# Optimization experiments

Hardware: AMD Instinct MI355X
Metric: run time of the kernel (lower is better)

## Reference

```python
import jax, jax.numpy as jnp
import numpy as np

H_STEP = 0.01  # Rosenbrock step size h


def phi_1_pade(A):
    """Pade(1,1) approximation of phi_1(z) = (e^z - 1)/z.

    phi_1(z) ~ (1 + z/6) / (1 - z/3), applied as a matrix function:
    (I - A/3)^{-1} (I + A/6). A: [..., d, d].
    """
    d = A.shape[-1]
    I = jnp.eye(d, dtype=A.dtype)
    return jnp.linalg.solve(I - A / 3.0, I + A / 6.0)


def setup_inputs() -> dict:
    key = jax.random.key(0)
    k_y, k_w1, k_w2 = jax.random.split(key, 3)
    B, D, HID = 512, 256, 1024
    y = jax.random.normal(k_y, (B, D), jnp.float32)
    W1 = jax.random.normal(k_w1, (HID, D), jnp.float32) / np.float32(np.sqrt(D))
    b1 = jnp.zeros((HID,), jnp.float32)
    W2 = jax.random.normal(k_w2, (D, HID), jnp.float32) / np.float32(np.sqrt(HID))
    b2 = jnp.zeros((D,), jnp.float32)
    return {"y": y, "W1": W1, "b1": b1, "W2": W2, "b2": b2}


def reference(y, W1, b1, W2, b2):
    dim = W2.shape[0]  # state dimension d

    def f(y_mu):  # SDE drift: 2-layer tanh MLP, R^d -> R^d
        return W2 @ jnp.tanh(W1 @ y_mu + b1) + b2

    def jac_and_val(y_mu):
        # jacfwd with aux: Jacobian and function value in one forward pass
        jac, val = jax.jacfwd(lambda z: (f(z), f(z)), has_aux=True)(y_mu)
        return jac, val

    y_mu = y[..., :dim]
    y_sigma = y[..., dim:]  # empty: y has exactly dim columns
    jac, y_mu_new = jax.vmap(jac_and_val)(y_mu)  # jac: [B, d, d]
    phi = phi_1_pade(H_STEP * jac)               # [B, d, d]
    combined = jnp.concatenate([y_mu_new, y_sigma], axis=-1)[..., None]  # [B, d, 1]
    return jnp.matmul(phi, combined)[..., 0]     # [B, d]
```

## Files before the change

### kernel.cpp

```cpp
#include <hip/hip_runtime.h>
#include <math.h>


#define B_SZ 512
#define D_SZ 256
#define HID_SZ 1024

typedef short short8 __attribute__((ext_vector_type(8)));
typedef float f32x4 __attribute__((ext_vector_type(4)));

__device__ __forceinline__ float bf16_to_f32(unsigned short u) {
    union { unsigned int i; float f; } c; c.i = ((unsigned int)u) << 16; return c.f;
}
__device__ __forceinline__ unsigned short f32_to_bf16(float f) {
    union { float f; unsigned int i; } c; c.f = f;
    unsigned int b = c.i + 0x7FFFu + ((c.i >> 16) & 1u);
    return (unsigned short)(b >> 16);
}

__global__ __launch_bounds__(256)
void prep_bf16(const float* __restrict__ Y, const float* __restrict__ W1,
               const float* __restrict__ W2, unsigned short* __restrict__ dst)
{
    int i8 = (blockIdx.x * 256 + threadIdx.x) * 8;
    const float* src; int off;
    if (i8 < 131072)      { src = Y;  off = i8; }
    else if (i8 < 393216) { src = W1; off = i8 - 131072; }
    else                  { src = W2; off = i8 - 393216; }
    float4 a = *(const float4*)&src[off];
    float4 b = *(const float4*)&src[off + 4];
    union { unsigned short u[8]; uint4 v; } o;
    o.u[0] = f32_to_bf16(a.x); o.u[1] = f32_to_bf16(a.y);
    o.u[2] = f32_to_bf16(a.z); o.u[3] = f32_to_bf16(a.w);
    o.u[4] = f32_to_bf16(b.x); o.u[5] = f32_to_bf16(b.y);
    o.u[6] = f32_to_bf16(b.z); o.u[7] = f32_to_bf16(b.w);
    *(uint4*)&dst[i8] = o.v;
}

enum { EPI_T = 0, EPI_P = 1 };
template<int EPI>
__global__ __launch_bounds__(256)
void gemm_h(const unsigned short* __restrict__ Ab,
            const unsigned short* __restrict__ Wb,
            const float* __restrict__ b1,
            const unsigned short* __restrict__ Tin,
            unsigned short* __restrict__ Ob)
{
    __shared__ alignas(16) unsigned short As[32][72];
    __shared__ alignas(16) unsigned short Bs[64][72];
    const int tid = threadIdx.x;
    const int bm = blockIdx.x * 32;
    const int bn = blockIdx.y * 64;
    const int wid = tid >> 6, lane = tid & 63;
    const int l16 = lane & 15, quad = lane >> 4;
    const int wm = wid >> 1, wn = wid & 1;

    f32x4 acc0 = {0.f, 0.f, 0.f, 0.f}, acc1 = {0.f, 0.f, 0.f, 0.f};
    const int arow = tid >> 3, acol = (tid & 7) * 8;

    for (int k0 = 0; k0 < 256; k0 += 64) {
        *(uint4*)&As[arow][acol] = *(const uint4*)&Ab[(size_t)(bm + arow) * 256 + k0 + acol];
#pragma unroll
        for (int r = 0; r < 2; ++r) {
            int u = r * 256 + tid;
            int brow = u >> 3, bcol = (u & 7) * 8;
            *(uint4*)&Bs[brow][bcol] = *(const uint4*)&Wb[(size_t)(bn + brow) * 256 + k0 + bcol];
        }
        __syncthreads();
#pragma unroll
        for (int ks = 0; ks < 64; ks += 32) {
            short8 a  = *(const short8*)&As[wm * 16 + l16][ks + quad * 8];
            short8 b0 = *(const short8*)&Bs[wn * 32 + l16][ks + quad * 8];
            short8 b1f = *(const short8*)&Bs[wn * 32 + 16 + l16][ks + quad * 8];
            acc0 = __builtin_amdgcn_mfma_f32_16x16x32_bf16(a, b0, acc0, 0, 0, 0);
            acc1 = __builtin_amdgcn_mfma_f32_16x16x32_bf16(a, b1f, acc1, 0, 0, 0);
        }
        __syncthreads();
    }
#pragma unroll
    for (int t2 = 0; t2 < 2; ++t2) {
        f32x4 acc = t2 ? acc1 : acc0;
        int col = bn + wn * 32 + t2 * 16 + l16;
        float bias = (EPI == EPI_T) ? b1[col] : 0.f;
#pragma unroll
        for (int r = 0; r < 4; ++r) {
            int row = bm + wm * 16 + quad * 4 + r;
            float v = acc[r];
            float o;
            if constexpr (EPI == EPI_T) {
                o = tanhf(v + bias);
            } else {
                float tt = bf16_to_f32(Tin[(size_t)row * 1024 + col]);
                o = v * (1.f - tt * tt);
            }
            Ob[(size_t)row * 1024 + col] = f32_to_bf16(o);
        }
    }
}

enum { EPI_V = 0, EPI_O = 1 };
template<int EPI>
__global__ __launch_bounds__(256)
void gemm_d(const unsigned short* __restrict__ Ab,
            const unsigned short* __restrict__ Wb,
            const float* __restrict__ b2,
            const float* __restrict__ Vf_in,
            float* __restrict__ Vf_out,
            unsigned short* __restrict__ Vb_out,
            float* __restrict__ OUT)
{
    __shared__ alignas(16) unsigned short As[4][16][72];
    __shared__ alignas(16) unsigned short Bs[4][32][72];
    __shared__ alignas(16) float red[4][16][34];
    const int tid = threadIdx.x;
    const int bm = blockIdx.x * 16;
    const int bn = blockIdx.y * 32;
    const int wid = tid >> 6, lane = tid & 63;
    const int l16 = lane & 15, quad = lane >> 4;

    f32x4 acc0 = {0.f, 0.f, 0.f, 0.f}, acc1 = {0.f, 0.f, 0.f, 0.f};

    for (int i = 0; i < 4; ++i) {
#pragma unroll
        for (int r = 0; r < 2; ++r) {
            int u = r * 256 + tid;
            int c = u >> 7, rem = u & 127;
            int row = rem >> 3, col = (rem & 7) * 8;
            *(uint4*)&As[c][row][col] =
                *(const uint4*)&Ab[(size_t)(bm + row) * 1024 + c * 256 + i * 64 + col];
        }
#pragma unroll
        for (int r = 0; r < 4; ++r) {
            int u = r * 256 + tid;
            int c = u >> 8, rem = u & 255;
            int row = rem >> 3, col = (rem & 7) * 8;
            *(uint4*)&Bs[c][row][col] =
                *(const uint4*)&Wb[(size_t)(bn + row) * 1024 + c * 256 + i * 64 + col];
        }
        __syncthreads();
#pragma unroll
        for (int ks = 0; ks < 64; ks += 32) {
            short8 a  = *(const short8*)&As[wid][l16][ks + quad * 8];
            short8 b0 = *(const short8*)&Bs[wid][l16][ks + quad * 8];
            short8 b1f = *(const short8*)&Bs[wid][16 + l16][ks + quad * 8];
            acc0 = __builtin_amdgcn_mfma_f32_16x16x32_bf16(a, b0, acc0, 0, 0, 0);
            acc1 = __builtin_amdgcn_mfma_f32_16x16x32_bf16(a, b1f, acc1, 0, 0, 0);
        }
        __syncthreads();
    }
#pragma unroll
    for (int r = 0; r < 4; ++r) {
        red[wid][quad * 4 + r][l16]      = acc0[r];
        red[wid][quad * 4 + r][16 + l16] = acc1[r];
    }
    __syncthreads();
    {
        int m = tid >> 4, n = (tid & 15) * 2;
        float2 s = {0.f, 0.f};
#pragma unroll
        for (int w = 0; w < 4; ++w) {
            float2 p = *(const float2*)&red[w][m][n];
            s.x += p.x; s.y += p.y;
        }
        int gm = bm + m, gn = bn + n;
        size_t idx = (size_t)gm * 256 + gn;
        if constexpr (EPI == EPI_V) {
            float2 bb = *(const float2*)&b2[gn];
            float2 v = {s.x + bb.x, s.y + bb.y};
            *(float2*)&Vf_out[idx] = v;
            Vb_out[idx]     = f32_to_bf16(v.x);
            Vb_out[idx + 1] = f32_to_bf16(v.y);
        } else {
            float2 vv = *(const float2*)&Vf_in[idx];
            float2 o = {fmaf(0.005f, s.x, vv.x), fmaf(0.005f, s.y, vv.y)};
            *(float2*)&OUT[idx] = o;
        }
    }
}

extern "C" void kernel_launch(void* const* d_in, const int* in_sizes, int n_in,
                              void* d_out, int out_size, void* d_ws, size_t ws_size,
                              hipStream_t stream) {
    const float* Y  = (const float*)d_in[0];
    const float* W1 = (const float*)d_in[1];
    const float* b1 = (const float*)d_in[2];
    const float* W2 = (const float*)d_in[3];
    const float* b2 = (const float*)d_in[4];
    float* OUT = (float*)d_out;

    unsigned short* wsu = (unsigned short*)d_ws;
    unsigned short* Yb  = wsu;
    unsigned short* W1b = wsu + 131072;
    unsigned short* W2b = wsu + 393216;
    unsigned short* Tb  = wsu + 655360;
    unsigned short* Pb  = wsu + 1179648;
    float*          Vf  = (float*)(wsu + 1703936);
    unsigned short* Vb  = wsu + 1966080;

    prep_bf16<<<320, 256, 0, stream>>>(Y, W1, W2, wsu);
    gemm_h<EPI_T><<<dim3(16, 16), 256, 0, stream>>>(Yb, W1b, b1, nullptr, Tb);
    gemm_d<EPI_V><<<dim3(32, 8), 256, 0, stream>>>(Tb, W2b, b2, nullptr, Vf, Vb, nullptr);
    gemm_h<EPI_P><<<dim3(16, 16), 256, 0, stream>>>(Vb, W1b, nullptr, Tb, Pb);
    gemm_d<EPI_O><<<dim3(32, 8), 256, 0, stream>>>(Pb, W2b, nullptr, Vf, nullptr, nullptr, OUT);
}
```

Measured before the change: 82.69 us.

## Fuse all stages into one persistent kernel with hierarchical grid barriers

Replaces the bf16 prep kernel and four GEMM launches with a single 256-block kernel. The stages are separated by a two-level atomic grid barrier, and operands are converted from fp32 to bf16 on the fly while loading into shared memory. This is meant to remove launch gaps and the separate conversion pass. In exchange it relies on all 256 blocks being co-resident, adds a memset and the barrier spin cost, and re-reads the fp32 weights in every stage instead of the smaller bf16 copies.

```diff
diff --git a/kernel.cpp b/kernel.cpp
--- a/kernel.cpp
+++ b/kernel.cpp
@@ -17,40 +17,48 @@
     unsigned int b = c.i + 0x7FFFu + ((c.i >> 16) & 1u);
     return (unsigned short)(b >> 16);
 }
-
-__global__ __launch_bounds__(256)
-void prep_bf16(const float* __restrict__ Y, const float* __restrict__ W1,
-               const float* __restrict__ W2, unsigned short* __restrict__ dst)
-{
-    int i8 = (blockIdx.x * 256 + threadIdx.x) * 8;
-    const float* src; int off;
-    if (i8 < 131072)      { src = Y;  off = i8; }
-    else if (i8 < 393216) { src = W1; off = i8 - 131072; }
-    else                  { src = W2; off = i8 - 393216; }
-    float4 a = *(const float4*)&src[off];
-    float4 b = *(const float4*)&src[off + 4];
+__device__ __forceinline__ uint4 pack8(float4 lo, float4 hi) {
     union { unsigned short u[8]; uint4 v; } o;
-    o.u[0] = f32_to_bf16(a.x); o.u[1] = f32_to_bf16(a.y);
-    o.u[2] = f32_to_bf16(a.z); o.u[3] = f32_to_bf16(a.w);
-    o.u[4] = f32_to_bf16(b.x); o.u[5] = f32_to_bf16(b.y);
-    o.u[6] = f32_to_bf16(b.z); o.u[7] = f32_to_bf16(b.w);
-    *(uint4*)&dst[i8] = o.v;
+    o.u[0] = f32_to_bf16(lo.x); o.u[1] = f32_to_bf16(lo.y);
+    o.u[2] = f32_to_bf16(lo.z); o.u[3] = f32_to_bf16(lo.w);
+    o.u[4] = f32_to_bf16(hi.x); o.u[5] = f32_to_bf16(hi.y);
+    o.u[6] = f32_to_bf16(hi.z); o.u[7] = f32_to_bf16(hi.w);
+    return o.v;
+}
+
+struct SMh { unsigned short A[32][72]; unsigned short B[64][72]; };
+struct SMd { unsigned short A[64][72]; unsigned short B[128][72]; float r[64][34]; };
+union SMu { SMh h; SMd d; };
+
+__device__ __forceinline__ void gbar(unsigned* c) {
+    __syncthreads();
+    if (threadIdx.x == 0) {
+        __threadfence();
+        unsigned* leaf = c + (blockIdx.x & 31) * 16;
+        unsigned* root = c + 32 * 16;
+        unsigned old = __hip_atomic_fetch_add(leaf, 1u, __ATOMIC_ACQ_REL,
+                                              __HIP_MEMORY_SCOPE_AGENT);
+        if (old == 7u)
+            __hip_atomic_fetch_add(root, 1u, __ATOMIC_ACQ_REL,
+                                   __HIP_MEMORY_SCOPE_AGENT);
+        while (__hip_atomic_load(root, __ATOMIC_ACQUIRE,
+                                 __HIP_MEMORY_SCOPE_AGENT) < 32u)
+            __builtin_amdgcn_s_sleep(2);
+        __threadfence();
+    }
+    __syncthreads();
 }
 
 enum { EPI_T = 0, EPI_P = 1 };
 template<int EPI>
-__global__ __launch_bounds__(256)
-void gemm_h(const unsigned short* __restrict__ Ab,
-            const unsigned short* __restrict__ Wb,
-            const float* __restrict__ b1,
-            const unsigned short* __restrict__ Tin,
-            unsigned short* __restrict__ Ob)
+__device__ __forceinline__
+void stage_h(SMh* sm, const float* __restrict__ Afp, const float* __restrict__ W1,
+             const float* __restrict__ b1, const unsigned short* __restrict__ Tin,
+             unsigned short* __restrict__ Ob)
 {
-    __shared__ alignas(16) unsigned short As[32][72];
-    __shared__ alignas(16) unsigned short Bs[64][72];
     const int tid = threadIdx.x;
-    const int bm = blockIdx.x * 32;
-    const int bn = blockIdx.y * 64;
+    const int bm = (blockIdx.x & 15) * 32;
+    const int bn = (blockIdx.x >> 4) * 64;
     const int wid = tid >> 6, lane = tid & 63;
     const int l16 = lane & 15, quad = lane >> 4;
     const int wm = wid >> 1, wn = wid & 1;
@@ -59,21 +67,29 @@
     const int arow = tid >> 3, acol = (tid & 7) * 8;
 
     for (int k0 = 0; k0 < 256; k0 += 64) {
-        *(uint4*)&As[arow][acol] = *(const uint4*)&Ab[(size_t)(bm + arow) * 256 + k0 + acol];
+        {
+            const float* src = &Afp[(size_t)(bm + arow) * 256 + k0 + acol];
+            float4 lo = *(const float4*)src;
+            float4 hi = *(const float4*)(src + 4);
+            *(uint4*)&sm->A[arow][acol] = pack8(lo, hi);
+        }
 #pragma unroll
         for (int r = 0; r < 2; ++r) {
             int u = r * 256 + tid;
             int brow = u >> 3, bcol = (u & 7) * 8;
-            *(uint4*)&Bs[brow][bcol] = *(const uint4*)&Wb[(size_t)(bn + brow) * 256 + k0 + bcol];
+            const float* src = &W1[(size_t)(bn + brow) * 256 + k0 + bcol];
+            float4 lo = *(const float4*)src;
+            float4 hi = *(const float4*)(src + 4);
+            *(uint4*)&sm->B[brow][bcol] = pack8(lo, hi);
         }
         __syncthreads();
 #pragma unroll
         for (int ks = 0; ks < 64; ks += 32) {
-            short8 a  = *(const short8*)&As[wm * 16 + l16][ks + quad * 8];
-            short8 b0 = *(const short8*)&Bs[wn * 32 + l16][ks + quad * 8];
-            short8 b1f = *(const short8*)&Bs[wn * 32 + 16 + l16][ks + quad * 8];
-            acc0 = __builtin_amdgcn_mfma_f32_16x16x32_bf16(a, b0, acc0, 0, 0, 0);
-            acc1 = __builtin_amdgcn_mfma_f32_16x16x32_bf16(a, b1f, acc1, 0, 0, 0);
+            short8 a   = *(const short8*)&sm->A[wm * 16 + l16][ks + quad * 8];
+            short8 b0  = *(const short8*)&sm->B[wn * 32 + l16][ks + quad * 8];
+            short8 b1v = *(const short8*)&sm->B[wn * 32 + 16 + l16][ks + quad * 8];
+            acc0 = __builtin_amdgcn_mfma_f32_16x16x32_bf16(a, b0,  acc0, 0, 0, 0);
+            acc1 = __builtin_amdgcn_mfma_f32_16x16x32_bf16(a, b1v, acc1, 0, 0, 0);
         }
         __syncthreads();
     }
@@ -81,7 +97,8 @@
     for (int t2 = 0; t2 < 2; ++t2) {
         f32x4 acc = t2 ? acc1 : acc0;
         int col = bn + wn * 32 + t2 * 16 + l16;
-        float bias = (EPI == EPI_T) ? b1[col] : 0.f;
+        float bias = 0.f;
+        if constexpr (EPI == EPI_T) bias = b1[col];
 #pragma unroll
         for (int r = 0; r < 4; ++r) {
             int row = bm + wm * 16 + quad * 4 + r;
@@ -100,21 +117,15 @@
 
 enum { EPI_V = 0, EPI_O = 1 };
 template<int EPI>
-__global__ __launch_bounds__(256)
-void gemm_d(const unsigned short* __restrict__ Ab,
-            const unsigned short* __restrict__ Wb,
-            const float* __restrict__ b2,
-            const float* __restrict__ Vf_in,
-            float* __restrict__ Vf_out,
-            unsigned short* __restrict__ Vb_out,
-            float* __restrict__ OUT)
+__device__ __forceinline__
+void stage_d(SMd* sm, const unsigned short* __restrict__ Ab,
+             const float* __restrict__ W2, const float* __restrict__ b2,
+             const float* __restrict__ Vin, float* __restrict__ Vout,
+             float* __restrict__ OUT)
 {
-    __shared__ alignas(16) unsigned short As[4][16][72];
-    __shared__ alignas(16) unsigned short Bs[4][32][72];
-    __shared__ alignas(16) float red[4][16][34];
     const int tid = threadIdx.x;
-    const int bm = blockIdx.x * 16;
-    const int bn = blockIdx.y * 32;
+    const int bm = (blockIdx.x & 31) * 16;
+    const int bn = (blockIdx.x >> 5) * 32;
     const int wid = tid >> 6, lane = tid & 63;
     const int l16 = lane & 15, quad = lane >> 4;
 
@@ -126,7 +137,7 @@
             int u = r * 256 + tid;
             int c = u >> 7, rem = u & 127;
             int row = rem >> 3, col = (rem & 7) * 8;
-            *(uint4*)&As[c][row][col] =
+            *(uint4*)&sm->A[c * 16 + row][col] =
                 *(const uint4*)&Ab[(size_t)(bm + row) * 1024 + c * 256 + i * 64 + col];
         }
 #pragma unroll
@@ -134,24 +145,26 @@
             int u = r * 256 + tid;
             int c = u >> 8, rem = u & 255;
             int row = rem >> 3, col = (rem & 7) * 8;
-            *(uint4*)&Bs[c][row][col] =
-                *(const uint4*)&Wb[(size_t)(bn + row) * 1024 + c * 256 + i * 64 + col];
+            const float* src = &W2[(size_t)(bn + row) * 1024 + c * 256 + i * 64 + col];
+            float4 lo = *(const float4*)src;
+            float4 hi = *(const float4*)(src + 4);
+            *(uint4*)&sm->B[c * 32 + row][col] = pack8(lo, hi);
         }
         __syncthreads();
 #pragma unroll
         for (int ks = 0; ks < 64; ks += 32) {
-            short8 a  = *(const short8*)&As[wid][l16][ks + quad * 8];
-            short8 b0 = *(const short8*)&Bs[wid][l16][ks + quad * 8];
-            short8 b1f = *(const short8*)&Bs[wid][16 + l16][ks + quad * 8];
-            acc0 = __builtin_amdgcn_mfma_f32_16x16x32_bf16(a, b0, acc0, 0, 0, 0);
-            acc1 = __builtin_amdgcn_mfma_f32_16x16x32_bf16(a, b1f, acc1, 0, 0, 0);
+            short8 a   = *(const short8*)&sm->A[wid * 16 + l16][ks + quad * 8];
+            short8 b0  = *(const short8*)&sm->B[wid * 32 + l16][ks + quad * 8];
+            short8 b1v = *(const short8*)&sm->B[wid * 32 + 16 + l16][ks + quad * 8];
+            acc0 = __builtin_amdgcn_mfma_f32_16x16x32_bf16(a, b0,  acc0, 0, 0, 0);
+            acc1 = __builtin_amdgcn_mfma_f32_16x16x32_bf16(a, b1v, acc1, 0, 0, 0);
         }
         __syncthreads();
     }
 #pragma unroll
     for (int r = 0; r < 4; ++r) {
-        red[wid][quad * 4 + r][l16]      = acc0[r];
-        red[wid][quad * 4 + r][16 + l16] = acc1[r];
+        sm->r[wid * 16 + quad * 4 + r][l16]      = acc0[r];
+        sm->r[wid * 16 + quad * 4 + r][16 + l16] = acc1[r];
     }
     __syncthreads();
     {
@@ -159,7 +172,7 @@
         float2 s = {0.f, 0.f};
 #pragma unroll
         for (int w = 0; w < 4; ++w) {
-            float2 p = *(const float2*)&red[w][m][n];
+            float2 p = *(const float2*)&sm->r[w * 16 + m][n];
             s.x += p.x; s.y += p.y;
         }
         int gm = bm + m, gn = bn + n;
@@ -167,15 +180,30 @@
         if constexpr (EPI == EPI_V) {
             float2 bb = *(const float2*)&b2[gn];
             float2 v = {s.x + bb.x, s.y + bb.y};
-            *(float2*)&Vf_out[idx] = v;
-            Vb_out[idx]     = f32_to_bf16(v.x);
-            Vb_out[idx + 1] = f32_to_bf16(v.y);
+            *(float2*)&Vout[idx] = v;
         } else {
-            float2 vv = *(const float2*)&Vf_in[idx];
+            float2 vv = *(const float2*)&Vin[idx];
             float2 o = {fmaf(0.005f, s.x, vv.x), fmaf(0.005f, s.y, vv.y)};
             *(float2*)&OUT[idx] = o;
         }
     }
+}
+
+__global__ __launch_bounds__(256)
+void fused_all(const float* __restrict__ Y, const float* __restrict__ W1,
+               const float* __restrict__ b1, const float* __restrict__ W2,
+               const float* __restrict__ b2, float* __restrict__ OUT,
+               unsigned short* __restrict__ Tb, unsigned short* __restrict__ Pb,
+               float* __restrict__ Vf, unsigned* __restrict__ bar)
+{
+    __shared__ alignas(16) SMu sm;
+    stage_h<EPI_T>(&sm.h, Y, W1, b1, nullptr, Tb);
+    gbar(bar);
+    stage_d<EPI_V>(&sm.d, Tb, W2, b2, nullptr, Vf, nullptr);
+    gbar(bar + 33 * 16);
+    stage_h<EPI_P>(&sm.h, Vf, W1, nullptr, Tb, Pb);
+    gbar(bar + 2 * 33 * 16);
+    stage_d<EPI_O>(&sm.d, Pb, W2, nullptr, Vf, nullptr, OUT);
 }
 
 extern "C" void kernel_launch(void* const* d_in, const int* in_sizes, int n_in,
@@ -188,18 +216,11 @@
     const float* b2 = (const float*)d_in[4];
     float* OUT = (float*)d_out;
 
-    unsigned short* wsu = (unsigned short*)d_ws;
-    unsigned short* Yb  = wsu;
-    unsigned short* W1b = wsu + 131072;
-    unsigned short* W2b = wsu + 393216;
-    unsigned short* Tb  = wsu + 655360;
-    unsigned short* Pb  = wsu + 1179648;
-    float*          Vf  = (float*)(wsu + 1703936);
-    unsigned short* Vb  = wsu + 1966080;
-
-    prep_bf16<<<320, 256, 0, stream>>>(Y, W1, W2, wsu);
-    gemm_h<EPI_T><<<dim3(16, 16), 256, 0, stream>>>(Yb, W1b, b1, nullptr, Tb);
-    gemm_d<EPI_V><<<dim3(32, 8), 256, 0, stream>>>(Tb, W2b, b2, nullptr, Vf, Vb, nullptr);
-    gemm_h<EPI_P><<<dim3(16, 16), 256, 0, stream>>>(Vb, W1b, nullptr, Tb, Pb);
-    gemm_d<EPI_O><<<dim3(32, 8), 256, 0, stream>>>(Pb, W2b, nullptr, Vf, nullptr, nullptr, OUT);
-}
+    unsigned* bar = (unsigned*)d_ws;
+    unsigned short* Tb = (unsigned short*)((char*)d_ws + 8192);
+    unsigned short* Pb = Tb + (size_t)B_SZ * HID_SZ;
+    float* Vf = (float*)(Pb + (size_t)B_SZ * HID_SZ);
+
+    hipMemsetAsync(d_ws, 0, 3 * 33 * 16 * sizeof(unsigned), stream);
+    fused_all<<<256, 256, 0, stream>>>(Y, W1, b1, W2, b2, OUT, Tb, Pb, Vf, bar);
+}
```

Result: slower. 150.8 us (+82.4%).
